# Performance work log

Measured on AMD Instinct MI355X. Metric: run time of the kernel, lower is better.

The kernel has to match this reference:

```python
import jax, jax.numpy as jnp
import numpy as np

B, S, H = 32, 2048, 512

def setup_inputs() -> dict:
    key = jax.random.key(0)
    k1, k2, k3, k4 = jax.random.split(key, 4)
    Y = jax.random.normal(k1, (B, S, H), dtype=jnp.float32)
    mask_Y = jnp.ones((B, S), dtype=jnp.float32)
    W = jax.random.normal(k2, (H, H), dtype=jnp.float32)
    b = jax.random.normal(k3, (H,), dtype=jnp.float32)
    w = jax.random.normal(k4, (H,), dtype=jnp.float32)
    return {"Y": Y, "mask_Y": mask_Y, "W": W, "b": b, "w": w}

def reference(Y, mask_Y, W, b, w):
    # u: [B,S,H] = tanh(Y @ W + b)
    u = jnp.tanh(jnp.einsum('bsh,hd->bsd', Y, W) + b)
    # scores: [B,S] = u . w, masked with large negative additive bias
    scores = jnp.einsum('bsh,h->bs', u, w) - 1000.0 * (1.0 - mask_Y)
    alpha = jax.nn.softmax(scores, axis=1)  # [B,S]
    # c_star: [B,H] = attention-weighted sum of Y
    c_star = jnp.einsum('bs,bsh->bh', alpha, Y)
    return c_star
```

## Files before the change

kernel.cpp:

```cpp
#include <hip/hip_runtime.h>
#include <hip/hip_bf16.h>


#define Bsz 32
#define Ssz 2048
#define Hsz 512
#define Msz (Bsz * Ssz)

using half8   = __attribute__((ext_vector_type(8))) _Float16;
using floatx4 = __attribute__((ext_vector_type(4))) float;

__device__ __forceinline__ void llds16(void* l, const void* g) {
  __builtin_amdgcn_global_load_lds((const __attribute__((address_space(1))) void*)g,
                                   (__attribute__((address_space(3))) void*)l, 16, 0, 0);
}

__device__ __forceinline__ float fast_tanh(float x) {
  const float e = __expf(2.f * x);
  return 1.f - 2.f / (e + 1.f);
}

__global__ __launch_bounds__(256) void wsplit_k(const float* __restrict__ W,
                                                _Float16* __restrict__ Wt) {
  __shared__ float tile[32][33];
  const int bx = blockIdx.x & 15, by = blockIdx.x >> 4;
  const int tx = threadIdx.x & 31, ty = threadIdx.x >> 5;
#pragma unroll
  for (int i = 0; i < 4; ++i)
    tile[ty + 8 * i][tx] = W[(size_t)(by * 32 + ty + 8 * i) * Hsz + bx * 32 + tx];
  __syncthreads();
#pragma unroll
  for (int i = 0; i < 4; ++i) {
    const int n = bx * 32 + ty + 8 * i;
    const int k = by * 32 + tx;
    Wt[(size_t)n * Hsz + k] = (_Float16)tile[tx][ty + 8 * i];
  }
}

__global__ __launch_bounds__(256) void gemm_score_k(const float* __restrict__ Y,
                                                    const _Float16* __restrict__ Wt,
                                                    const float* __restrict__ bvec,
                                                    const float* __restrict__ wvec,
                                                    float* __restrict__ scores4) {
  __shared__ __align__(16) float    As[128 * 32];
  __shared__ __align__(16) _Float16 Bs[128 * 32];
  const int tid = threadIdx.x;
  const int lane = tid & 63, wv = tid >> 6;
  const int wr = wv >> 1, wc = wv & 1;
  const int lr = lane & 15, lq = lane >> 4;
  const int g = blockIdx.x;
  const int x = g & 7, q = g >> 3;
  const int nblk = q & 3;
  const int mblk = (q >> 2) * 8 + x;

  floatx4 acc[4][4];
#pragma unroll
  for (int rf = 0; rf < 4; ++rf)
#pragma unroll
    for (int cf = 0; cf < 4; ++cf)
      acc[rf][cf] = (floatx4){0.f, 0.f, 0.f, 0.f};

  const float* aY = Y + (size_t)mblk * 128 * Hsz;
  const _Float16* bW = Wt + (size_t)nblk * 128 * Hsz;

  for (int it = 0; it < 16; ++it) {
    const int k0 = it * 32;
#pragma unroll
    for (int i = 0; i < 4; ++i) {
      const int cb = i * 256 + wv * 64;
      const int p = cb + lane;
      const int row = p >> 3;
      const int gc = (p & 7) ^ (row & 7);
      llds16(&As[cb * 4], aY + (size_t)row * Hsz + k0 + gc * 4);
    }
#pragma unroll
    for (int i = 0; i < 2; ++i) {
      const int cb = i * 256 + wv * 64;
      const int p = cb + lane;
      const int row = p >> 2;
      const int gc = (p & 3) ^ ((row >> 1) & 3);
      llds16(&Bs[cb * 8], bW + (size_t)row * Hsz + k0 + gc * 8);
    }
    __syncthreads();

    half8 a[4], bf[4];
#pragma unroll
    for (int rf = 0; rf < 4; ++rf) {
      const int ar = wr * 64 + rf * 16 + lr;
      const int s0 = (lq * 2) ^ (ar & 7);
      const float4 flo = *(const float4*)&As[ar * 32 + s0 * 4];
      const float4 fhi = *(const float4*)&As[ar * 32 + (s0 ^ 1) * 4];
      half8 h;
      h[0] = (_Float16)flo.x; h[1] = (_Float16)flo.y;
      h[2] = (_Float16)flo.z; h[3] = (_Float16)flo.w;
      h[4] = (_Float16)fhi.x; h[5] = (_Float16)fhi.y;
      h[6] = (_Float16)fhi.z; h[7] = (_Float16)fhi.w;
      a[rf] = h;
    }
#pragma unroll
    for (int cf = 0; cf < 4; ++cf) {
      const int nr = wc * 64 + cf * 16 + lr;
      bf[cf] = *(const half8*)&Bs[nr * 32 + (lq ^ ((nr >> 1) & 3)) * 8];
    }
#pragma unroll
    for (int rf = 0; rf < 4; ++rf)
#pragma unroll
      for (int cf = 0; cf < 4; ++cf)
        acc[rf][cf] = __builtin_amdgcn_mfma_f32_16x16x32_f16(a[rf], bf[cf], acc[rf][cf], 0, 0, 0);
    __syncthreads();
  }

  float bb[4], ww[4];
  const int colbase = nblk * 128 + wc * 64;
#pragma unroll
  for (int cf = 0; cf < 4; ++cf) {
    const int col = colbase + cf * 16 + lr;
    bb[cf] = bvec[col];
    ww[cf] = wvec[col];
  }
  float* red = (float*)As;
#pragma unroll
  for (int rf = 0; rf < 4; ++rf) {
#pragma unroll
    for (int r = 0; r < 4; ++r) {
      float v = 0.f;
#pragma unroll
      for (int cf = 0; cf < 4; ++cf)
        v += fast_tanh(acc[rf][cf][r] + bb[cf]) * ww[cf];
      v += __shfl_xor(v, 1, 16);
      v += __shfl_xor(v, 2, 16);
      v += __shfl_xor(v, 4, 16);
      v += __shfl_xor(v, 8, 16);
      if (lr == 0)
        red[(wr * 64 + rf * 16 + lq * 4 + r) * 2 + wc] = v;
    }
  }
  __syncthreads();
  if (tid < 128)
    scores4[(size_t)nblk * Msz + mblk * 128 + tid] = red[2 * tid] + red[2 * tid + 1];
}

__global__ __launch_bounds__(256) void softmax_k(const float* __restrict__ scores4,
                                                 const float* __restrict__ mask,
                                                 float* __restrict__ alpha) {
  const int b = blockIdx.x, t = threadIdx.x;
  const int lane = t & 63, wv = t >> 6;
  float s[8];
  float mx = -3.4e38f;
#pragma unroll
  for (int i = 0; i < 8; ++i) {
    const int idx = b * Ssz + i * 256 + t;
    float v = scores4[idx] + scores4[Msz + idx] + scores4[2 * Msz + idx] + scores4[3 * Msz + idx];
    v -= 1000.f * (1.f - mask[idx]);
    s[i] = v;
    mx = fmaxf(mx, v);
  }
  for (int off = 32; off > 0; off >>= 1) mx = fmaxf(mx, __shfl_xor(mx, off, 64));
  __shared__ float rm[4], rs[4];
  if (lane == 0) rm[wv] = mx;
  __syncthreads();
  mx = fmaxf(fmaxf(rm[0], rm[1]), fmaxf(rm[2], rm[3]));
  float sum = 0.f;
#pragma unroll
  for (int i = 0; i < 8; ++i) {
    s[i] = __expf(s[i] - mx);
    sum += s[i];
  }
  for (int off = 32; off > 0; off >>= 1) sum += __shfl_xor(sum, off, 64);
  if (lane == 0) rs[wv] = sum;
  __syncthreads();
  sum = rs[0] + rs[1] + rs[2] + rs[3];
  const float inv = 1.f / sum;
#pragma unroll
  for (int i = 0; i < 8; ++i) alpha[b * Ssz + i * 256 + t] = s[i] * inv;
}

__global__ __launch_bounds__(256) void wsum1_k(const float* __restrict__ alpha,
                                               const float* __restrict__ Y,
                                               float* __restrict__ partial) {
  const int b = blockIdx.x >> 5, sc = blockIdx.x & 31;
  const int t = threadIdx.x, lane = t & 63, wv = t >> 6;
  __shared__ float part[4 * 512];
  const int s0 = sc * 64 + wv * 16;
  const float* al = alpha + b * Ssz + s0;
  const float4* Yb = (const float4*)(Y + ((size_t)b * Ssz + s0) * Hsz);
  float a0 = 0.f, a1 = 0.f, a2 = 0.f, a3 = 0.f, a4 = 0.f, a5 = 0.f, a6 = 0.f, a7 = 0.f;
#pragma unroll 4
  for (int r = 0; r < 16; ++r) {
    const float a = al[r];
    const float4 y0 = Yb[r * 128 + lane * 2];
    const float4 y1 = Yb[r * 128 + lane * 2 + 1];
    a0 = fmaf(a, y0.x, a0); a1 = fmaf(a, y0.y, a1);
    a2 = fmaf(a, y0.z, a2); a3 = fmaf(a, y0.w, a3);
    a4 = fmaf(a, y1.x, a4); a5 = fmaf(a, y1.y, a5);
    a6 = fmaf(a, y1.z, a6); a7 = fmaf(a, y1.w, a7);
  }
  part[wv * 512 + 0 * 64 + lane] = a0;
  part[wv * 512 + 1 * 64 + lane] = a1;
  part[wv * 512 + 2 * 64 + lane] = a2;
  part[wv * 512 + 3 * 64 + lane] = a3;
  part[wv * 512 + 4 * 64 + lane] = a4;
  part[wv * 512 + 5 * 64 + lane] = a5;
  part[wv * 512 + 6 * 64 + lane] = a6;
  part[wv * 512 + 7 * 64 + lane] = a7;
  __syncthreads();
#pragma unroll
  for (int i = 0; i < 2; ++i) {
    const int h = i * 256 + t;
    const int idx = (h & 7) * 64 + (h >> 3);
    partial[((size_t)(b * 32 + sc)) * Hsz + h] =
        part[idx] + part[512 + idx] + part[1024 + idx] + part[1536 + idx];
  }
}

__global__ __launch_bounds__(256) void wsum2_k(const float* __restrict__ partial,
                                               float* __restrict__ out) {
  const int b = blockIdx.x >> 1;
  const int h = (blockIdx.x & 1) * 256 + threadIdx.x;
  float s = 0.f;
#pragma unroll 8
  for (int sc = 0; sc < 32; ++sc)
    s += partial[((size_t)(b * 32 + sc)) * Hsz + h];
  out[b * Hsz + h] = s;
}

extern "C" void kernel_launch(void* const* d_in, const int* in_sizes, int n_in,
                              void* d_out, int out_size, void* d_ws, size_t ws_size,
                              hipStream_t stream) {
  (void)in_sizes; (void)n_in; (void)out_size; (void)ws_size;
  const float* Y    = (const float*)d_in[0];
  const float* mask = (const float*)d_in[1];
  const float* W    = (const float*)d_in[2];
  const float* bvec = (const float*)d_in[3];
  const float* wvec = (const float*)d_in[4];
  float* out = (float*)d_out;

  char* ws = (char*)d_ws;
  _Float16* Wt   = (_Float16*)ws;
  float* scores4 = (float*)(ws + ((size_t)1 << 20));
  float* alpha   = (float*)(ws + ((size_t)2 << 20));
  float* partial = (float*)(ws + ((size_t)3 << 20));

  wsplit_k<<<256, 256, 0, stream>>>(W, Wt);
  gemm_score_k<<<(Msz / 128) * 4, 256, 0, stream>>>(Y, Wt, bvec, wvec, scores4);
  softmax_k<<<Bsz, 256, 0, stream>>>(scores4, mask, alpha);
  wsum1_k<<<Bsz * 32, 256, 0, stream>>>(alpha, Y, partial);
  wsum2_k<<<Bsz * 2, 256, 0, stream>>>(partial, out);
}
```

Measured before the change: 273.1 us.

## Keep W slice resident in LDS and stream Y rows directly into MFMA

The GEMM kernel is restructured so each block loads a full 64-column slice of the fp16 W (64x512) into LDS once, in MFMA fragment order. It then loops over 8 row blocks, reading Y straight from global memory into registers with no LDS staging and no per-k-step barriers. The N split grows from 4 to 8 partial score buffers, so the softmax now sums 8 partials and the workspace offsets shift to fit. This removes the repeated W reloads and the sync overhead, at the cost of 64 KB of LDS per block and Y loads with no latency hiding beyond occupancy. Y is now read 8 times instead of 4, which raises global traffic.

```diff
diff --git a/kernel.cpp b/kernel.cpp
--- a/kernel.cpp
+++ b/kernel.cpp
@@ -37,107 +37,91 @@
   }
 }
 
-__global__ __launch_bounds__(256) void gemm_score_k(const float* __restrict__ Y,
-                                                    const _Float16* __restrict__ Wt,
-                                                    const float* __restrict__ bvec,
-                                                    const float* __restrict__ wvec,
-                                                    float* __restrict__ scores4) {
-  __shared__ __align__(16) float    As[128 * 32];
-  __shared__ __align__(16) _Float16 Bs[128 * 32];
+__global__ __launch_bounds__(256, 2) void gemm_score_k(const float* __restrict__ Y,
+                                                       const _Float16* __restrict__ Wt,
+                                                       const float* __restrict__ bvec,
+                                                       const float* __restrict__ wvec,
+                                                       float* __restrict__ scores4) {
+  __shared__ __align__(16) _Float16 Bs[64 * 512];
   const int tid = threadIdx.x;
   const int lane = tid & 63, wv = tid >> 6;
-  const int wr = wv >> 1, wc = wv & 1;
   const int lr = lane & 15, lq = lane >> 4;
-  const int g = blockIdx.x;
-  const int x = g & 7, q = g >> 3;
-  const int nblk = q & 3;
-  const int mblk = (q >> 2) * 8 + x;
-
-  floatx4 acc[4][4];
-#pragma unroll
-  for (int rf = 0; rf < 4; ++rf)
-#pragma unroll
-    for (int cf = 0; cf < 4; ++cf)
-      acc[rf][cf] = (floatx4){0.f, 0.f, 0.f, 0.f};
-
-  const float* aY = Y + (size_t)mblk * 128 * Hsz;
-  const _Float16* bW = Wt + (size_t)nblk * 128 * Hsz;
-
-  for (int it = 0; it < 16; ++it) {
-    const int k0 = it * 32;
-#pragma unroll
-    for (int i = 0; i < 4; ++i) {
-      const int cb = i * 256 + wv * 64;
-      const int p = cb + lane;
-      const int row = p >> 3;
-      const int gc = (p & 7) ^ (row & 7);
-      llds16(&As[cb * 4], aY + (size_t)row * Hsz + k0 + gc * 4);
-    }
-#pragma unroll
-    for (int i = 0; i < 2; ++i) {
-      const int cb = i * 256 + wv * 64;
-      const int p = cb + lane;
-      const int row = p >> 2;
-      const int gc = (p & 3) ^ ((row >> 1) & 3);
-      llds16(&Bs[cb * 8], bW + (size_t)row * Hsz + k0 + gc * 8);
-    }
-    __syncthreads();
-
-    half8 a[4], bf[4];
-#pragma unroll
-    for (int rf = 0; rf < 4; ++rf) {
-      const int ar = wr * 64 + rf * 16 + lr;
-      const int s0 = (lq * 2) ^ (ar & 7);
-      const float4 flo = *(const float4*)&As[ar * 32 + s0 * 4];
-      const float4 fhi = *(const float4*)&As[ar * 32 + (s0 ^ 1) * 4];
-      half8 h;
-      h[0] = (_Float16)flo.x; h[1] = (_Float16)flo.y;
-      h[2] = (_Float16)flo.z; h[3] = (_Float16)flo.w;
-      h[4] = (_Float16)fhi.x; h[5] = (_Float16)fhi.y;
-      h[6] = (_Float16)fhi.z; h[7] = (_Float16)fhi.w;
-      a[rf] = h;
-    }
-#pragma unroll
-    for (int cf = 0; cf < 4; ++cf) {
-      const int nr = wc * 64 + cf * 16 + lr;
-      bf[cf] = *(const half8*)&Bs[nr * 32 + (lq ^ ((nr >> 1) & 3)) * 8];
-    }
-#pragma unroll
-    for (int rf = 0; rf < 4; ++rf)
-#pragma unroll
-      for (int cf = 0; cf < 4; ++cf)
-        acc[rf][cf] = __builtin_amdgcn_mfma_f32_16x16x32_f16(a[rf], bf[cf], acc[rf][cf], 0, 0, 0);
-    __syncthreads();
-  }
+  const int c = blockIdx.x;
+  const int x = c & 7, grp = c >> 3;
+  const int nblk = grp & 7;
+  const int mbase = x * 64 + (grp >> 3) * 8;
+
+  const _Float16* bW = Wt + (size_t)nblk * 64 * Hsz;
+
+#pragma unroll
+  for (int i = 0; i < 16; ++i) {
+    const int fb = wv * 16 + i;
+    const int ks = fb >> 2, cf = fb & 3;
+    llds16(&Bs[(size_t)fb * 512],
+           bW + (size_t)(cf * 16 + lr) * Hsz + ks * 32 + lq * 8);
+  }
+  __syncthreads();
 
   float bb[4], ww[4];
-  const int colbase = nblk * 128 + wc * 64;
 #pragma unroll
   for (int cf = 0; cf < 4; ++cf) {
-    const int col = colbase + cf * 16 + lr;
+    const int col = nblk * 64 + cf * 16 + lr;
     bb[cf] = bvec[col];
     ww[cf] = wvec[col];
   }
-  float* red = (float*)As;
-#pragma unroll
-  for (int rf = 0; rf < 4; ++rf) {
-#pragma unroll
-    for (int r = 0; r < 4; ++r) {
-      float v = 0.f;
+
+  for (int m = 0; m < 8; ++m) {
+    const int mblk = mbase + m;
+    const float* aRow0 = Y + (size_t)(mblk * 128 + wv * 32 + lr) * Hsz + lq * 8;
+    const float* aRow1 = aRow0 + (size_t)16 * Hsz;
+
+    floatx4 acc[2][4];
+#pragma unroll
+    for (int rf = 0; rf < 2; ++rf)
 #pragma unroll
       for (int cf = 0; cf < 4; ++cf)
-        v += fast_tanh(acc[rf][cf][r] + bb[cf]) * ww[cf];
-      v += __shfl_xor(v, 1, 16);
-      v += __shfl_xor(v, 2, 16);
-      v += __shfl_xor(v, 4, 16);
-      v += __shfl_xor(v, 8, 16);
-      if (lr == 0)
-        red[(wr * 64 + rf * 16 + lq * 4 + r) * 2 + wc] = v;
+        acc[rf][cf] = (floatx4){0.f, 0.f, 0.f, 0.f};
+
+#pragma unroll
+    for (int ks = 0; ks < 16; ++ks) {
+      const float4 f00 = *(const float4*)(aRow0 + ks * 32);
+      const float4 f01 = *(const float4*)(aRow0 + ks * 32 + 4);
+      const float4 f10 = *(const float4*)(aRow1 + ks * 32);
+      const float4 f11 = *(const float4*)(aRow1 + ks * 32 + 4);
+      half8 a0, a1;
+      a0[0] = (_Float16)f00.x; a0[1] = (_Float16)f00.y;
+      a0[2] = (_Float16)f00.z; a0[3] = (_Float16)f00.w;
+      a0[4] = (_Float16)f01.x; a0[5] = (_Float16)f01.y;
+      a0[6] = (_Float16)f01.z; a0[7] = (_Float16)f01.w;
+      a1[0] = (_Float16)f10.x; a1[1] = (_Float16)f10.y;
+      a1[2] = (_Float16)f10.z; a1[3] = (_Float16)f10.w;
+      a1[4] = (_Float16)f11.x; a1[5] = (_Float16)f11.y;
+      a1[6] = (_Float16)f11.z; a1[7] = (_Float16)f11.w;
+#pragma unroll
+      for (int cf = 0; cf < 4; ++cf) {
+        const half8 bf = *(const half8*)&Bs[(size_t)(ks * 4 + cf) * 512 + lane * 8];
+        acc[0][cf] = __builtin_amdgcn_mfma_f32_16x16x32_f16(a0, bf, acc[0][cf], 0, 0, 0);
+        acc[1][cf] = __builtin_amdgcn_mfma_f32_16x16x32_f16(a1, bf, acc[1][cf], 0, 0, 0);
+      }
     }
-  }
-  __syncthreads();
-  if (tid < 128)
-    scores4[(size_t)nblk * Msz + mblk * 128 + tid] = red[2 * tid] + red[2 * tid + 1];
+
+#pragma unroll
+    for (int rf = 0; rf < 2; ++rf) {
+#pragma unroll
+      for (int r = 0; r < 4; ++r) {
+        float v = 0.f;
+#pragma unroll
+        for (int cf = 0; cf < 4; ++cf)
+          v += fast_tanh(acc[rf][cf][r] + bb[cf]) * ww[cf];
+        v += __shfl_xor(v, 1, 16);
+        v += __shfl_xor(v, 2, 16);
+        v += __shfl_xor(v, 4, 16);
+        v += __shfl_xor(v, 8, 16);
+        if (lr == 0)
+          scores4[(size_t)nblk * Msz + mblk * 128 + wv * 32 + rf * 16 + lq * 4 + r] = v;
+      }
+    }
+  }
 }
 
 __global__ __launch_bounds__(256) void softmax_k(const float* __restrict__ scores4,
@@ -150,7 +134,9 @@
 #pragma unroll
   for (int i = 0; i < 8; ++i) {
     const int idx = b * Ssz + i * 256 + t;
-    float v = scores4[idx] + scores4[Msz + idx] + scores4[2 * Msz + idx] + scores4[3 * Msz + idx];
+    float v = 0.f;
+#pragma unroll
+    for (int p = 0; p < 8; ++p) v += scores4[(size_t)p * Msz + idx];
     v -= 1000.f * (1.f - mask[idx]);
     s[i] = v;
     mx = fmaxf(mx, v);
@@ -237,12 +223,12 @@
 
   char* ws = (char*)d_ws;
   _Float16* Wt   = (_Float16*)ws;
-  float* scores4 = (float*)(ws + ((size_t)1 << 20));
-  float* alpha   = (float*)(ws + ((size_t)2 << 20));
+  float* scores4 = (float*)(ws + ((size_t)512 << 10));
+  float* alpha   = (float*)(ws + ((size_t)2560 << 10));
   float* partial = (float*)(ws + ((size_t)3 << 20));
 
   wsplit_k<<<256, 256, 0, stream>>>(W, Wt);
-  gemm_score_k<<<(Msz / 128) * 4, 256, 0, stream>>>(Y, Wt, bvec, wvec, scores4);
+  gemm_score_k<<<512, 256, 0, stream>>>(Y, Wt, bvec, wvec, scores4);
   softmax_k<<<Bsz, 256, 0, stream>>>(scores4, mask, alpha);
   wsum1_k<<<Bsz * 32, 256, 0, stream>>>(alpha, Y, partial);
   wsum2_k<<<Bsz * 2, 256, 0, stream>>>(partial, out);
```

After: 451.0 us. +65.1%, slower.
